# Kernel optimization log

Hardware: AMD Instinct MI355X
Metric: run time of the kernel (lower is better)

Reference implementation:

```python
import jax, jax.numpy as jnp
import numpy as np

N_NODES = 100000
N_EDGES = 3200000
NODE_DIM = 128
HIDDEN = 16


def setup_inputs() -> dict:
    key = jax.random.key(0)
    ks = jax.random.split(key, 12)
    x = jax.random.normal(ks[0], (N_NODES, NODE_DIM), dtype=jnp.float32)
    edge_src = jax.random.randint(ks[1], (N_EDGES,), 0, N_NODES, dtype=jnp.int32)
    edge_dst = jax.random.randint(ks[2], (N_EDGES,), 0, N_NODES, dtype=jnp.int32)
    # QCNN block params (Linear(node_dim,16), Linear(16,16), Linear(16,16)) + classifier Linear(16,1)
    s1 = 1.0 / np.sqrt(NODE_DIM)
    s2 = 1.0 / np.sqrt(HIDDEN)
    W1 = jax.random.uniform(ks[3], (NODE_DIM, HIDDEN), jnp.float32, -s1, s1)
    b1 = jax.random.uniform(ks[4], (HIDDEN,), jnp.float32, -s1, s1)
    W2 = jax.random.uniform(ks[5], (HIDDEN, HIDDEN), jnp.float32, -s2, s2)
    b2 = jax.random.uniform(ks[6], (HIDDEN,), jnp.float32, -s2, s2)
    W3 = jax.random.uniform(ks[7], (HIDDEN, HIDDEN), jnp.float32, -s2, s2)
    b3 = jax.random.uniform(ks[8], (HIDDEN,), jnp.float32, -s2, s2)
    Wc = jax.random.uniform(ks[9], (HIDDEN, 1), jnp.float32, -s2, s2)
    bc = jax.random.uniform(ks[10], (1,), jnp.float32, -s2, s2)
    return {"x": x, "edge_src": edge_src, "edge_dst": edge_dst,
            "W1": W1, "b1": b1, "W2": W2, "b2": b2, "W3": W3, "b3": b3,
            "Wc": Wc, "bc": bc}


def reference(x, edge_src, edge_dst, W1, b1, W2, b2, W3, b3, Wc, bc):
    # per-node tiny 3-layer tanh MLP (QCNN block), vectorized over all nodes
    h = jnp.tanh(x @ W1 + b1)
    h = jnp.tanh(h @ W2 + b2)
    h = jnp.tanh(h @ W3 + b3)  # [N, H]
    n = x.shape[0]
    # degree of each aggregating node; nodes with no neighbors contribute 0
    deg = jnp.zeros((n,), x.dtype).at[edge_src].add(1.0)
    inv_deg = jnp.where(deg > 0, 1.0 / jnp.maximum(deg, 1.0), 0.0)
    # aggregated = sum_n mean_{m in N(n)} h[m] = sum_e h[dst_e] / deg[src_e]
    agg = jnp.sum(h[edge_dst] * inv_deg[edge_src][:, None], axis=0) / n  # [H]
    return jax.nn.sigmoid(agg @ Wc + bc)  # [1]
```

## Files before the change

### kernel.cpp

```cpp
#include <hip/hip_runtime.h>
#include <math.h>


#define NODE_DIM 128
#define HID 16

typedef __attribute__((ext_vector_type(8))) short    bfrag8;
typedef __attribute__((ext_vector_type(4))) _Float16 hfrag4;
typedef __attribute__((ext_vector_type(4))) float    f32x4;

__device__ __forceinline__ float fast_tanh(float x) {
    x = fminf(fmaxf(x, -10.0f), 10.0f);
    float e = __expf(2.0f * x);
    return (e - 1.0f) * __frcp_rn(e + 1.0f);
}
__device__ __forceinline__ unsigned short f2bf(float f) {
    unsigned u = __float_as_uint(f);
    return (unsigned short)((u + 0x7FFFu + ((u >> 16) & 1u)) >> 16);
}

__global__ __launch_bounds__(256) void k_mlp(
    const float* __restrict__ x,
    const float* __restrict__ W1, const float* __restrict__ b1,
    const float* __restrict__ W2, const float* __restrict__ b2,
    const float* __restrict__ W3, const float* __restrict__ b3,
    const float* __restrict__ Wc,
    unsigned char* __restrict__ c_code, int n_nodes)
{
    const int lane = threadIdx.x & 63;
    const int col  = lane & 15;
    const int q    = lane >> 4;

    bfrag8 w1f[4];
#pragma unroll
    for (int kc = 0; kc < 4; ++kc)
#pragma unroll
        for (int j = 0; j < 8; ++j)
            w1f[kc][j] = (short)f2bf(W1[(kc * 32 + q * 8 + j) * HID + col]);

    hfrag4 w2t, w3t;
#pragma unroll
    for (int j = 0; j < 4; ++j) {
        w2t[j] = (_Float16)W2[(q * 4 + j) * HID + col];
        w3t[j] = (_Float16)W3[(q * 4 + j) * HID + col];
    }
    float bb1[4], bb2[4], bb3[4], wcr[4];
#pragma unroll
    for (int j = 0; j < 4; ++j) {
        bb1[j] = b1[q * 4 + j]; bb2[j] = b2[q * 4 + j];
        bb3[j] = b3[q * 4 + j]; wcr[j] = Wc[q * 4 + j];
    }

    const int ngroups = (n_nodes + 15) >> 4;
    const int nwaves  = gridDim.x * (blockDim.x >> 6);
    const int wgid    = (blockIdx.x * blockDim.x + threadIdx.x) >> 6;
    const f32x4 zero = {0.f, 0.f, 0.f, 0.f};

    for (int g = wgid; g < ngroups; g += nwaves) {
        const int node0 = g << 4;
        int m = node0 + col;
        int mload = (m < n_nodes) ? m : (n_nodes - 1);
        const float* xr = x + (size_t)mload * NODE_DIM;

        float4 xa[4], xb[4];
#pragma unroll
        for (int kc = 0; kc < 4; ++kc) {
            const float* p = xr + kc * 32 + q * 8;
            xa[kc] = *reinterpret_cast<const float4*>(p);
            xb[kc] = *reinterpret_cast<const float4*>(p + 4);
        }
        f32x4 d1 = zero;
#pragma unroll
        for (int kc = 0; kc < 4; ++kc) {
            bfrag8 bf;
            bf[0] = (short)f2bf(xa[kc].x); bf[1] = (short)f2bf(xa[kc].y);
            bf[2] = (short)f2bf(xa[kc].z); bf[3] = (short)f2bf(xa[kc].w);
            bf[4] = (short)f2bf(xb[kc].x); bf[5] = (short)f2bf(xb[kc].y);
            bf[6] = (short)f2bf(xb[kc].z); bf[7] = (short)f2bf(xb[kc].w);
            d1 = __builtin_amdgcn_mfma_f32_16x16x32_bf16(w1f[kc], bf, d1, 0, 0, 0);
        }
        hfrag4 h1;
#pragma unroll
        for (int r = 0; r < 4; ++r) h1[r] = (_Float16)fast_tanh(d1[r] + bb1[r]);

        f32x4 d2 = __builtin_amdgcn_mfma_f32_16x16x16f16(w2t, h1, zero, 0, 0, 0);
        hfrag4 h2;
#pragma unroll
        for (int r = 0; r < 4; ++r) h2[r] = (_Float16)fast_tanh(d2[r] + bb2[r]);

        f32x4 d3 = __builtin_amdgcn_mfma_f32_16x16x16f16(w3t, h2, zero, 0, 0, 0);

        float v = 0.0f;
#pragma unroll
        for (int r = 0; r < 4; ++r) v += fast_tanh(d3[r] + bb3[r]) * wcr[r];
        v += __shfl_xor(v, 16, 64);
        v += __shfl_xor(v, 32, 64);

        if (lane < 16) {
            const int node = node0 + lane;
            if (node < n_nodes) {
                float c = fminf(fmaxf(v, -4.0f), 4.0f);
                c_code[node] = (unsigned char)__float2int_rn((c + 4.0f) * 16.0f);
            }
        }
    }
}

__global__ __launch_bounds__(1024) void k_gaccum(
    const int* __restrict__ src, const int* __restrict__ dst,
    const unsigned char* __restrict__ c_code,
    unsigned int* __restrict__ tables,
    float* __restrict__ gtotal, unsigned int* __restrict__ ticket,
    int n_edges, int ch, int n_chunks, int n_slices)
{
    extern __shared__ unsigned char dynlds[];
    unsigned int* tab = (unsigned int*)dynlds;
    const int tid   = threadIdx.x;
    const int chunk = blockIdx.x % n_chunks;
    const int slice = blockIdx.x / n_chunks;
    const int lo    = chunk * ch;
    const int words = ch >> 1;

    if (blockIdx.x == 0 && tid == 0) { *gtotal = 0.0f; *ticket = 0u; }

    uint4* t4 = reinterpret_cast<uint4*>(tab);
    const uint4 z4 = {0u, 0u, 0u, 0u};
    for (int i = tid; i < (words >> 2); i += 1024) t4[i] = z4;
    __syncthreads();

    const int epb = ((n_edges + n_slices - 1) / n_slices + 7) & ~7;
    const int e0 = slice * epb;
    const int e1 = min(e0 + epb, n_edges);

    for (int e = e0 + (tid << 3); e < e1; e += 1024 * 8) {
        if (e + 7 < e1) {
            int4 s0 = *reinterpret_cast<const int4*>(src + e);
            int4 s1 = *reinterpret_cast<const int4*>(src + e + 4);
            int4 d0 = *reinterpret_cast<const int4*>(dst + e);
            int4 d1 = *reinterpret_cast<const int4*>(dst + e + 4);
            unsigned c0 = c_code[d0.x], c1 = c_code[d0.y];
            unsigned c2 = c_code[d0.z], c3 = c_code[d0.w];
            unsigned c4 = c_code[d1.x], c5 = c_code[d1.y];
            unsigned c6 = c_code[d1.z], c7 = c_code[d1.w];
            int i0 = s0.x - lo, i1 = s0.y - lo, i2 = s0.z - lo, i3 = s0.w - lo;
            int i4 = s1.x - lo, i5 = s1.y - lo, i6 = s1.z - lo, i7 = s1.w - lo;
            if ((unsigned)i0 < (unsigned)ch) atomicAdd(&tab[i0 >> 1], ((1u << 12) | c0) << ((i0 & 1) << 4));
            if ((unsigned)i1 < (unsigned)ch) atomicAdd(&tab[i1 >> 1], ((1u << 12) | c1) << ((i1 & 1) << 4));
            if ((unsigned)i2 < (unsigned)ch) atomicAdd(&tab[i2 >> 1], ((1u << 12) | c2) << ((i2 & 1) << 4));
            if ((unsigned)i3 < (unsigned)ch) atomicAdd(&tab[i3 >> 1], ((1u << 12) | c3) << ((i3 & 1) << 4));
            if ((unsigned)i4 < (unsigned)ch) atomicAdd(&tab[i4 >> 1], ((1u << 12) | c4) << ((i4 & 1) << 4));
            if ((unsigned)i5 < (unsigned)ch) atomicAdd(&tab[i5 >> 1], ((1u << 12) | c5) << ((i5 & 1) << 4));
            if ((unsigned)i6 < (unsigned)ch) atomicAdd(&tab[i6 >> 1], ((1u << 12) | c6) << ((i6 & 1) << 4));
            if ((unsigned)i7 < (unsigned)ch) atomicAdd(&tab[i7 >> 1], ((1u << 12) | c7) << ((i7 & 1) << 4));
        } else {
            for (int j = e; j < e1; ++j) {
                int ss = src[j] - lo;
                if ((unsigned)ss < (unsigned)ch)
                    atomicAdd(&tab[ss >> 1],
                              ((1u << 12) | (unsigned)c_code[dst[j]]) << ((ss & 1) << 4));
            }
        }
    }
    __syncthreads();
    uint4* out4 = reinterpret_cast<uint4*>(tables + (size_t)(slice * n_chunks + chunk) * words);
    for (int i = tid; i < (words >> 2); i += 1024) out4[i] = t4[i];
}

__global__ __launch_bounds__(256) void k_totalfinal(
    const unsigned int* __restrict__ tables, const float* __restrict__ bc,
    float* __restrict__ out, float* __restrict__ gtotal,
    unsigned int* __restrict__ ticket,
    int n_chunks, int ch, int n_slices, float inv_n, int ntb)
{
    __shared__ float swave[4];
    const int wpc = ch >> 1;
    const int wg  = blockIdx.x * blockDim.x + threadIdx.x;
    const int chunk = wg / wpc, w = wg - chunk * wpc;
    const unsigned int stride = (unsigned int)(n_chunks * wpc);
    const unsigned int base0  = (unsigned int)(chunk * wpc + w);

    unsigned int sfix = 0, scnt = 0;
    for (int s = 0; s < n_slices; s += 8) {
        unsigned int v[8];
#pragma unroll
        for (int k = 0; k < 8; ++k)
            v[k] = tables[(size_t)(s + k) * stride + base0];
#pragma unroll
        for (int k = 0; k < 8; ++k) {
            sfix += v[k] & 0x0FFF0FFFu;
            scnt += (v[k] >> 12) & 0x000F000Fu;
        }
    }
    const unsigned int cnt_lo = scnt & 0xFFFFu, cnt_hi = scnt >> 16;
    const unsigned int fix_lo = sfix & 0xFFFFu, fix_hi = sfix >> 16;
    float contrib = 0.0f;
    if (cnt_lo > 0) contrib += (float)fix_lo / (16.0f * (float)cnt_lo) - 4.0f;
    if (cnt_hi > 0) contrib += (float)fix_hi / (16.0f * (float)cnt_hi) - 4.0f;

    for (int off = 32; off > 0; off >>= 1) contrib += __shfl_down(contrib, off, 64);
    if ((threadIdx.x & 63) == 0) swave[threadIdx.x >> 6] = contrib;
    __syncthreads();
    if (threadIdx.x == 0) {
        float part = swave[0] + swave[1] + swave[2] + swave[3];
        atomicAdd(gtotal, part);
        __threadfence();
        unsigned int t = atomicAdd(ticket, 1u);
        if (t == (unsigned int)(ntb - 1)) {
            __threadfence();
            float tot = atomicAdd(gtotal, 0.0f);
            float sv = tot * inv_n + bc[0];
            out[0] = 1.0f / (1.0f + __expf(-sv));
        }
    }
}

extern "C" void kernel_launch(void* const* d_in, const int* in_sizes, int n_in,
                              void* d_out, int out_size, void* d_ws, size_t ws_size,
                              hipStream_t stream) {
    const float* x   = (const float*)d_in[0];
    const int* esrc  = (const int*)d_in[1];
    const int* edst  = (const int*)d_in[2];
    const float* W1  = (const float*)d_in[3];
    const float* b1  = (const float*)d_in[4];
    const float* W2  = (const float*)d_in[5];
    const float* b2  = (const float*)d_in[6];
    const float* W3  = (const float*)d_in[7];
    const float* b3  = (const float*)d_in[8];
    const float* Wc  = (const float*)d_in[9];
    const float* bc  = (const float*)d_in[10];

    const int n_nodes = in_sizes[0] / NODE_DIM;
    const int n_edges = in_sizes[1];

    bool big = true;
    if (hipFuncSetAttribute((const void*)k_gaccum,
            hipFuncAttributeMaxDynamicSharedMemorySize, 131072) != hipSuccess) big = false;

    const int ch_a  = big ? 50176 : 32768;
    const int nch_a = (n_nodes + ch_a - 1) / ch_a;
    const int nsl   = 128;
    const int words = ch_a >> 1;

    const size_t tab_b = (size_t)nsl * nch_a * words * 4;
    unsigned int* tables  = (unsigned int*)d_ws;
    float* gtotal         = (float*)((char*)d_ws + tab_b);
    unsigned int* ticket  = (unsigned int*)(gtotal + 1);
    unsigned char* c_code = (unsigned char*)d_ws + tab_b + 16;

    k_mlp<<<512, 256, 0, stream>>>(x, W1, b1, W2, b2, W3, b3, Wc, c_code, n_nodes);

    k_gaccum<<<nsl * nch_a, 1024, (size_t)ch_a * 2, stream>>>(
        esrc, edst, c_code, tables, gtotal, ticket, n_edges, ch_a, nch_a, nsl);

    const int ntb = (nch_a * words) / 256;
    k_totalfinal<<<ntb, 256, 0, stream>>>(
        tables, bc, (float*)d_out, gtotal, ticket,
        nch_a, ch_a, nsl, 1.0f / (float)n_nodes, ntb);
}
```

Measured before the change: 152.6 us.

## Replace sliced LDS histogram tables with direct global per-node atomics

The chunked LDS histogram, which wrote 128 per-slice partial tables to global memory and then reduced them, is replaced by one packed 32-bit word per node (count in the upper half, quantized code sum in the lower half). Edges update these words with global atomics, and the final kernel reads one word per node. Zeroing of that table moves into the MLP kernel, which now launches one wave per 16-node group and issues the x loads before the weight loads. This removes the large partial-table write and readback, and the repeated edge scans per chunk. In exchange, all updates become random global atomics that contend in L2.

```diff
diff --git a/kernel.cpp b/kernel.cpp
--- a/kernel.cpp
+++ b/kernel.cpp
@@ -25,12 +25,39 @@
     const float* __restrict__ W2, const float* __restrict__ b2,
     const float* __restrict__ W3, const float* __restrict__ b3,
     const float* __restrict__ Wc,
-    unsigned char* __restrict__ c_code, int n_nodes)
+    unsigned char* __restrict__ c_code,
+    unsigned int* __restrict__ ntab,
+    float* __restrict__ gtotal, unsigned int* __restrict__ ticket,
+    int n_nodes)
 {
+    {
+        const int gsz = gridDim.x * blockDim.x;
+        for (int i = blockIdx.x * blockDim.x + threadIdx.x; i < n_nodes; i += gsz)
+            ntab[i] = 0u;
+        if (blockIdx.x == 0 && threadIdx.x == 0) { *gtotal = 0.0f; *ticket = 0u; }
+    }
+
     const int lane = threadIdx.x & 63;
     const int col  = lane & 15;
     const int q    = lane >> 4;
 
+    const int ngroups = (n_nodes + 15) >> 4;
+    const int wgid    = (blockIdx.x * blockDim.x + threadIdx.x) >> 6;
+    if (wgid >= ngroups) return;
+
+    const int node0 = wgid << 4;
+    int m = node0 + col;
+    int mload = (m < n_nodes) ? m : (n_nodes - 1);
+    const float* xr = x + (size_t)mload * NODE_DIM;
+
+    float4 xa[4], xb[4];
+#pragma unroll
+    for (int kc = 0; kc < 4; ++kc) {
+        const float* p = xr + kc * 32 + q * 8;
+        xa[kc] = *reinterpret_cast<const float4*>(p);
+        xb[kc] = *reinterpret_cast<const float4*>(p + 4);
+    }
+
     bfrag8 w1f[4];
 #pragma unroll
     for (int kc = 0; kc < 4; ++kc)
@@ -51,151 +78,90 @@
         bb3[j] = b3[q * 4 + j]; wcr[j] = Wc[q * 4 + j];
     }
 
-    const int ngroups = (n_nodes + 15) >> 4;
-    const int nwaves  = gridDim.x * (blockDim.x >> 6);
-    const int wgid    = (blockIdx.x * blockDim.x + threadIdx.x) >> 6;
     const f32x4 zero = {0.f, 0.f, 0.f, 0.f};
-
-    for (int g = wgid; g < ngroups; g += nwaves) {
-        const int node0 = g << 4;
-        int m = node0 + col;
-        int mload = (m < n_nodes) ? m : (n_nodes - 1);
-        const float* xr = x + (size_t)mload * NODE_DIM;
-
-        float4 xa[4], xb[4];
-#pragma unroll
-        for (int kc = 0; kc < 4; ++kc) {
-            const float* p = xr + kc * 32 + q * 8;
-            xa[kc] = *reinterpret_cast<const float4*>(p);
-            xb[kc] = *reinterpret_cast<const float4*>(p + 4);
+    f32x4 d1 = zero;
+#pragma unroll
+    for (int kc = 0; kc < 4; ++kc) {
+        bfrag8 bf;
+        bf[0] = (short)f2bf(xa[kc].x); bf[1] = (short)f2bf(xa[kc].y);
+        bf[2] = (short)f2bf(xa[kc].z); bf[3] = (short)f2bf(xa[kc].w);
+        bf[4] = (short)f2bf(xb[kc].x); bf[5] = (short)f2bf(xb[kc].y);
+        bf[6] = (short)f2bf(xb[kc].z); bf[7] = (short)f2bf(xb[kc].w);
+        d1 = __builtin_amdgcn_mfma_f32_16x16x32_bf16(w1f[kc], bf, d1, 0, 0, 0);
+    }
+    hfrag4 h1;
+#pragma unroll
+    for (int r = 0; r < 4; ++r) h1[r] = (_Float16)fast_tanh(d1[r] + bb1[r]);
+
+    f32x4 d2 = __builtin_amdgcn_mfma_f32_16x16x16f16(w2t, h1, zero, 0, 0, 0);
+    hfrag4 h2;
+#pragma unroll
+    for (int r = 0; r < 4; ++r) h2[r] = (_Float16)fast_tanh(d2[r] + bb2[r]);
+
+    f32x4 d3 = __builtin_amdgcn_mfma_f32_16x16x16f16(w3t, h2, zero, 0, 0, 0);
+
+    float v = 0.0f;
+#pragma unroll
+    for (int r = 0; r < 4; ++r) v += fast_tanh(d3[r] + bb3[r]) * wcr[r];
+    v += __shfl_xor(v, 16, 64);
+    v += __shfl_xor(v, 32, 64);
+
+    if (lane < 16) {
+        const int node = node0 + lane;
+        if (node < n_nodes) {
+            float c = fminf(fmaxf(v, -4.0f), 4.0f);
+            c_code[node] = (unsigned char)__float2int_rn((c + 4.0f) * 16.0f);
         }
-        f32x4 d1 = zero;
-#pragma unroll
-        for (int kc = 0; kc < 4; ++kc) {
-            bfrag8 bf;
-            bf[0] = (short)f2bf(xa[kc].x); bf[1] = (short)f2bf(xa[kc].y);
-            bf[2] = (short)f2bf(xa[kc].z); bf[3] = (short)f2bf(xa[kc].w);
-            bf[4] = (short)f2bf(xb[kc].x); bf[5] = (short)f2bf(xb[kc].y);
-            bf[6] = (short)f2bf(xb[kc].z); bf[7] = (short)f2bf(xb[kc].w);
-            d1 = __builtin_amdgcn_mfma_f32_16x16x32_bf16(w1f[kc], bf, d1, 0, 0, 0);
-        }
-        hfrag4 h1;
-#pragma unroll
-        for (int r = 0; r < 4; ++r) h1[r] = (_Float16)fast_tanh(d1[r] + bb1[r]);
-
-        f32x4 d2 = __builtin_amdgcn_mfma_f32_16x16x16f16(w2t, h1, zero, 0, 0, 0);
-        hfrag4 h2;
-#pragma unroll
-        for (int r = 0; r < 4; ++r) h2[r] = (_Float16)fast_tanh(d2[r] + bb2[r]);
-
-        f32x4 d3 = __builtin_amdgcn_mfma_f32_16x16x16f16(w3t, h2, zero, 0, 0, 0);
-
-        float v = 0.0f;
-#pragma unroll
-        for (int r = 0; r < 4; ++r) v += fast_tanh(d3[r] + bb3[r]) * wcr[r];
-        v += __shfl_xor(v, 16, 64);
-        v += __shfl_xor(v, 32, 64);
-
-        if (lane < 16) {
-            const int node = node0 + lane;
-            if (node < n_nodes) {
-                float c = fminf(fmaxf(v, -4.0f), 4.0f);
-                c_code[node] = (unsigned char)__float2int_rn((c + 4.0f) * 16.0f);
-            }
-        }
-    }
-}
-
-__global__ __launch_bounds__(1024) void k_gaccum(
+    }
+}
+
+__global__ __launch_bounds__(256) void k_edge(
     const int* __restrict__ src, const int* __restrict__ dst,
     const unsigned char* __restrict__ c_code,
-    unsigned int* __restrict__ tables,
-    float* __restrict__ gtotal, unsigned int* __restrict__ ticket,
-    int n_edges, int ch, int n_chunks, int n_slices)
+    unsigned int* __restrict__ ntab, int n_edges)
 {
-    extern __shared__ unsigned char dynlds[];
-    unsigned int* tab = (unsigned int*)dynlds;
-    const int tid   = threadIdx.x;
-    const int chunk = blockIdx.x % n_chunks;
-    const int slice = blockIdx.x / n_chunks;
-    const int lo    = chunk * ch;
-    const int words = ch >> 1;
-
-    if (blockIdx.x == 0 && tid == 0) { *gtotal = 0.0f; *ticket = 0u; }
-
-    uint4* t4 = reinterpret_cast<uint4*>(tab);
-    const uint4 z4 = {0u, 0u, 0u, 0u};
-    for (int i = tid; i < (words >> 2); i += 1024) t4[i] = z4;
-    __syncthreads();
-
-    const int epb = ((n_edges + n_slices - 1) / n_slices + 7) & ~7;
-    const int e0 = slice * epb;
-    const int e1 = min(e0 + epb, n_edges);
-
-    for (int e = e0 + (tid << 3); e < e1; e += 1024 * 8) {
-        if (e + 7 < e1) {
-            int4 s0 = *reinterpret_cast<const int4*>(src + e);
-            int4 s1 = *reinterpret_cast<const int4*>(src + e + 4);
-            int4 d0 = *reinterpret_cast<const int4*>(dst + e);
-            int4 d1 = *reinterpret_cast<const int4*>(dst + e + 4);
-            unsigned c0 = c_code[d0.x], c1 = c_code[d0.y];
-            unsigned c2 = c_code[d0.z], c3 = c_code[d0.w];
-            unsigned c4 = c_code[d1.x], c5 = c_code[d1.y];
-            unsigned c6 = c_code[d1.z], c7 = c_code[d1.w];
-            int i0 = s0.x - lo, i1 = s0.y - lo, i2 = s0.z - lo, i3 = s0.w - lo;
-            int i4 = s1.x - lo, i5 = s1.y - lo, i6 = s1.z - lo, i7 = s1.w - lo;
-            if ((unsigned)i0 < (unsigned)ch) atomicAdd(&tab[i0 >> 1], ((1u << 12) | c0) << ((i0 & 1) << 4));
-            if ((unsigned)i1 < (unsigned)ch) atomicAdd(&tab[i1 >> 1], ((1u << 12) | c1) << ((i1 & 1) << 4));
-            if ((unsigned)i2 < (unsigned)ch) atomicAdd(&tab[i2 >> 1], ((1u << 12) | c2) << ((i2 & 1) << 4));
-            if ((unsigned)i3 < (unsigned)ch) atomicAdd(&tab[i3 >> 1], ((1u << 12) | c3) << ((i3 & 1) << 4));
-            if ((unsigned)i4 < (unsigned)ch) atomicAdd(&tab[i4 >> 1], ((1u << 12) | c4) << ((i4 & 1) << 4));
-            if ((unsigned)i5 < (unsigned)ch) atomicAdd(&tab[i5 >> 1], ((1u << 12) | c5) << ((i5 & 1) << 4));
-            if ((unsigned)i6 < (unsigned)ch) atomicAdd(&tab[i6 >> 1], ((1u << 12) | c6) << ((i6 & 1) << 4));
-            if ((unsigned)i7 < (unsigned)ch) atomicAdd(&tab[i7 >> 1], ((1u << 12) | c7) << ((i7 & 1) << 4));
-        } else {
-            for (int j = e; j < e1; ++j) {
-                int ss = src[j] - lo;
-                if ((unsigned)ss < (unsigned)ch)
-                    atomicAdd(&tab[ss >> 1],
-                              ((1u << 12) | (unsigned)c_code[dst[j]]) << ((ss & 1) << 4));
-            }
-        }
-    }
-    __syncthreads();
-    uint4* out4 = reinterpret_cast<uint4*>(tables + (size_t)(slice * n_chunks + chunk) * words);
-    for (int i = tid; i < (words >> 2); i += 1024) out4[i] = t4[i];
-}
-
-__global__ __launch_bounds__(256) void k_totalfinal(
-    const unsigned int* __restrict__ tables, const float* __restrict__ bc,
+    const int t  = blockIdx.x * blockDim.x + threadIdx.x;
+    const int e  = t << 3;
+    if (e >= n_edges) return;
+
+    if (e + 7 < n_edges) {
+        int4 s0 = *reinterpret_cast<const int4*>(src + e);
+        int4 s1 = *reinterpret_cast<const int4*>(src + e + 4);
+        int4 d0 = *reinterpret_cast<const int4*>(dst + e);
+        int4 d1 = *reinterpret_cast<const int4*>(dst + e + 4);
+        unsigned c0 = c_code[d0.x], c1 = c_code[d0.y];
+        unsigned c2 = c_code[d0.z], c3 = c_code[d0.w];
+        unsigned c4 = c_code[d1.x], c5 = c_code[d1.y];
+        unsigned c6 = c_code[d1.z], c7 = c_code[d1.w];
+        atomicAdd(&ntab[s0.x], 0x10000u | c0);
+        atomicAdd(&ntab[s0.y], 0x10000u | c1);
+        atomicAdd(&ntab[s0.z], 0x10000u | c2);
+        atomicAdd(&ntab[s0.w], 0x10000u | c3);
+        atomicAdd(&ntab[s1.x], 0x10000u | c4);
+        atomicAdd(&ntab[s1.y], 0x10000u | c5);
+        atomicAdd(&ntab[s1.z], 0x10000u | c6);
+        atomicAdd(&ntab[s1.w], 0x10000u | c7);
+    } else {
+        for (int j = e; j < n_edges; ++j)
+            atomicAdd(&ntab[src[j]], 0x10000u | (unsigned)c_code[dst[j]]);
+    }
+}
+
+__global__ __launch_bounds__(256) void k_final(
+    const unsigned int* __restrict__ ntab, const float* __restrict__ bc,
     float* __restrict__ out, float* __restrict__ gtotal,
     unsigned int* __restrict__ ticket,
-    int n_chunks, int ch, int n_slices, float inv_n, int ntb)
+    int n_nodes, float inv_n, int nblocks)
 {
     __shared__ float swave[4];
-    const int wpc = ch >> 1;
-    const int wg  = blockIdx.x * blockDim.x + threadIdx.x;
-    const int chunk = wg / wpc, w = wg - chunk * wpc;
-    const unsigned int stride = (unsigned int)(n_chunks * wpc);
-    const unsigned int base0  = (unsigned int)(chunk * wpc + w);
-
-    unsigned int sfix = 0, scnt = 0;
-    for (int s = 0; s < n_slices; s += 8) {
-        unsigned int v[8];
-#pragma unroll
-        for (int k = 0; k < 8; ++k)
-            v[k] = tables[(size_t)(s + k) * stride + base0];
-#pragma unroll
-        for (int k = 0; k < 8; ++k) {
-            sfix += v[k] & 0x0FFF0FFFu;
-            scnt += (v[k] >> 12) & 0x000F000Fu;
-        }
-    }
-    const unsigned int cnt_lo = scnt & 0xFFFFu, cnt_hi = scnt >> 16;
-    const unsigned int fix_lo = sfix & 0xFFFFu, fix_hi = sfix >> 16;
+    const int i = blockIdx.x * blockDim.x + threadIdx.x;
+
     float contrib = 0.0f;
-    if (cnt_lo > 0) contrib += (float)fix_lo / (16.0f * (float)cnt_lo) - 4.0f;
-    if (cnt_hi > 0) contrib += (float)fix_hi / (16.0f * (float)cnt_hi) - 4.0f;
+    if (i < n_nodes) {
+        unsigned int w = ntab[i];
+        unsigned int cnt = w >> 16, fix = w & 0xFFFFu;
+        if (cnt > 0) contrib = (float)fix / (16.0f * (float)cnt) - 4.0f;
+    }
 
     for (int off = 32; off > 0; off >>= 1) contrib += __shfl_down(contrib, off, 64);
     if ((threadIdx.x & 63) == 0) swave[threadIdx.x >> 6] = contrib;
@@ -205,7 +171,7 @@
         atomicAdd(gtotal, part);
         __threadfence();
         unsigned int t = atomicAdd(ticket, 1u);
-        if (t == (unsigned int)(ntb - 1)) {
+        if (t == (unsigned int)(nblocks - 1)) {
             __threadfence();
             float tot = atomicAdd(gtotal, 0.0f);
             float sv = tot * inv_n + bc[0];
@@ -232,28 +198,21 @@
     const int n_nodes = in_sizes[0] / NODE_DIM;
     const int n_edges = in_sizes[1];
 
-    bool big = true;
-    if (hipFuncSetAttribute((const void*)k_gaccum,
-            hipFuncAttributeMaxDynamicSharedMemorySize, 131072) != hipSuccess) big = false;
-
-    const int ch_a  = big ? 50176 : 32768;
-    const int nch_a = (n_nodes + ch_a - 1) / ch_a;
-    const int nsl   = 128;
-    const int words = ch_a >> 1;
-
-    const size_t tab_b = (size_t)nsl * nch_a * words * 4;
-    unsigned int* tables  = (unsigned int*)d_ws;
-    float* gtotal         = (float*)((char*)d_ws + tab_b);
+    unsigned int* ntab    = (unsigned int*)d_ws;
+    float* gtotal         = (float*)(ntab + n_nodes);
     unsigned int* ticket  = (unsigned int*)(gtotal + 1);
-    unsigned char* c_code = (unsigned char*)d_ws + tab_b + 16;
-
-    k_mlp<<<512, 256, 0, stream>>>(x, W1, b1, W2, b2, W3, b3, Wc, c_code, n_nodes);
-
-    k_gaccum<<<nsl * nch_a, 1024, (size_t)ch_a * 2, stream>>>(
-        esrc, edst, c_code, tables, gtotal, ticket, n_edges, ch_a, nch_a, nsl);
-
-    const int ntb = (nch_a * words) / 256;
-    k_totalfinal<<<ntb, 256, 0, stream>>>(
-        tables, bc, (float*)d_out, gtotal, ticket,
-        nch_a, ch_a, nsl, 1.0f / (float)n_nodes, ntb);
-}
+    unsigned char* c_code = (unsigned char*)d_ws + (size_t)n_nodes * 4 + 16;
+
+    const int ngroups = (n_nodes + 15) >> 4;
+    const int mlp_wg  = (ngroups + 3) >> 2;
+    k_mlp<<<mlp_wg, 256, 0, stream>>>(x, W1, b1, W2, b2, W3, b3, Wc,
+                                      c_code, ntab, gtotal, ticket, n_nodes);
+
+    const int edge_blocks = (((n_edges + 7) >> 3) + 255) >> 8;
+    k_edge<<<edge_blocks, 256, 0, stream>>>(esrc, edst, c_code, ntab, n_edges);
+
+    const int fin_blocks = (n_nodes + 255) >> 8;
+    k_final<<<fin_blocks, 256, 0, stream>>>(ntab, bc, (float*)d_out,
+                                            gtotal, ticket, n_nodes,
+                                            1.0f / (float)n_nodes, fin_blocks);
+}
```

Result: slower. 261.3 us (+71.2%).

## Stage node codes in LDS for edge pass and retile chunks and slices

Applied to the files above, without the earlier changes.

The edge accumulation kernel now copies the whole per-node byte code array (about 100KB) into LDS, so the random gathers by dst index hit LDS instead of global memory or L2. To make room, LDS is raised to 160KB and the source-node range is split into 4 chunks × 64 slices, which also changes the partial-table layout. The MLP kernel becomes one-shot with one 16-node group per wave instead of a grid-stride loop, and the zeroing of gtotal and ticket moves into it. The tradeoff is that every block reloads the full code array, and occupancy is limited to one block per CU because of the large LDS footprint.

```diff
diff --git a/kernel.cpp b/kernel.cpp
--- a/kernel.cpp
+++ b/kernel.cpp
@@ -25,12 +25,33 @@
     const float* __restrict__ W2, const float* __restrict__ b2,
     const float* __restrict__ W3, const float* __restrict__ b3,
     const float* __restrict__ Wc,
-    unsigned char* __restrict__ c_code, int n_nodes)
+    unsigned char* __restrict__ c_code,
+    float* __restrict__ gtotal, unsigned int* __restrict__ ticket,
+    int n_nodes)
 {
+    if (blockIdx.x == 0 && threadIdx.x == 0) { *gtotal = 0.0f; *ticket = 0u; }
+
     const int lane = threadIdx.x & 63;
     const int col  = lane & 15;
     const int q    = lane >> 4;
 
+    const int ngroups = (n_nodes + 15) >> 4;
+    const int wgid    = (blockIdx.x * blockDim.x + threadIdx.x) >> 6;
+    if (wgid >= ngroups) return;
+
+    const int node0 = wgid << 4;
+    int m = node0 + col;
+    int mload = (m < n_nodes) ? m : (n_nodes - 1);
+    const float* xr = x + (size_t)mload * NODE_DIM;
+
+    float4 xa[4], xb[4];
+#pragma unroll
+    for (int kc = 0; kc < 4; ++kc) {
+        const float* p = xr + kc * 32 + q * 8;
+        xa[kc] = *reinterpret_cast<const float4*>(p);
+        xb[kc] = *reinterpret_cast<const float4*>(p + 4);
+    }
+
     bfrag8 w1f[4];
 #pragma unroll
     for (int kc = 0; kc < 4; ++kc)
@@ -51,78 +72,61 @@
         bb3[j] = b3[q * 4 + j]; wcr[j] = Wc[q * 4 + j];
     }
 
-    const int ngroups = (n_nodes + 15) >> 4;
-    const int nwaves  = gridDim.x * (blockDim.x >> 6);
-    const int wgid    = (blockIdx.x * blockDim.x + threadIdx.x) >> 6;
     const f32x4 zero = {0.f, 0.f, 0.f, 0.f};
-
-    for (int g = wgid; g < ngroups; g += nwaves) {
-        const int node0 = g << 4;
-        int m = node0 + col;
-        int mload = (m < n_nodes) ? m : (n_nodes - 1);
-        const float* xr = x + (size_t)mload * NODE_DIM;
-
-        float4 xa[4], xb[4];
-#pragma unroll
-        for (int kc = 0; kc < 4; ++kc) {
-            const float* p = xr + kc * 32 + q * 8;
-            xa[kc] = *reinterpret_cast<const float4*>(p);
-            xb[kc] = *reinterpret_cast<const float4*>(p + 4);
-        }
-        f32x4 d1 = zero;
-#pragma unroll
-        for (int kc = 0; kc < 4; ++kc) {
-            bfrag8 bf;
-            bf[0] = (short)f2bf(xa[kc].x); bf[1] = (short)f2bf(xa[kc].y);
-            bf[2] = (short)f2bf(xa[kc].z); bf[3] = (short)f2bf(xa[kc].w);
-            bf[4] = (short)f2bf(xb[kc].x); bf[5] = (short)f2bf(xb[kc].y);
-            bf[6] = (short)f2bf(xb[kc].z); bf[7] = (short)f2bf(xb[kc].w);
-            d1 = __builtin_amdgcn_mfma_f32_16x16x32_bf16(w1f[kc], bf, d1, 0, 0, 0);
-        }
-        hfrag4 h1;
-#pragma unroll
-        for (int r = 0; r < 4; ++r) h1[r] = (_Float16)fast_tanh(d1[r] + bb1[r]);
-
-        f32x4 d2 = __builtin_amdgcn_mfma_f32_16x16x16f16(w2t, h1, zero, 0, 0, 0);
-        hfrag4 h2;
-#pragma unroll
-        for (int r = 0; r < 4; ++r) h2[r] = (_Float16)fast_tanh(d2[r] + bb2[r]);
-
-        f32x4 d3 = __builtin_amdgcn_mfma_f32_16x16x16f16(w3t, h2, zero, 0, 0, 0);
-
-        float v = 0.0f;
-#pragma unroll
-        for (int r = 0; r < 4; ++r) v += fast_tanh(d3[r] + bb3[r]) * wcr[r];
-        v += __shfl_xor(v, 16, 64);
-        v += __shfl_xor(v, 32, 64);
-
-        if (lane < 16) {
-            const int node = node0 + lane;
-            if (node < n_nodes) {
-                float c = fminf(fmaxf(v, -4.0f), 4.0f);
-                c_code[node] = (unsigned char)__float2int_rn((c + 4.0f) * 16.0f);
-            }
-        }
-    }
-}
-
-__global__ __launch_bounds__(1024) void k_gaccum(
+    f32x4 d1 = zero;
+#pragma unroll
+    for (int kc = 0; kc < 4; ++kc) {
+        bfrag8 bf;
+        bf[0] = (short)f2bf(xa[kc].x); bf[1] = (short)f2bf(xa[kc].y);
+        bf[2] = (short)f2bf(xa[kc].z); bf[3] = (short)f2bf(xa[kc].w);
+        bf[4] = (short)f2bf(xb[kc].x); bf[5] = (short)f2bf(xb[kc].y);
+        bf[6] = (short)f2bf(xb[kc].z); bf[7] = (short)f2bf(xb[kc].w);
+        d1 = __builtin_amdgcn_mfma_f32_16x16x32_bf16(w1f[kc], bf, d1, 0, 0, 0);
+    }
+    hfrag4 h1;
+#pragma unroll
+    for (int r = 0; r < 4; ++r) h1[r] = (_Float16)fast_tanh(d1[r] + bb1[r]);
+
+    f32x4 d2 = __builtin_amdgcn_mfma_f32_16x16x16f16(w2t, h1, zero, 0, 0, 0);
+    hfrag4 h2;
+#pragma unroll
+    for (int r = 0; r < 4; ++r) h2[r] = (_Float16)fast_tanh(d2[r] + bb2[r]);
+
+    f32x4 d3 = __builtin_amdgcn_mfma_f32_16x16x16f16(w3t, h2, zero, 0, 0, 0);
+
+    float v = 0.0f;
+#pragma unroll
+    for (int r = 0; r < 4; ++r) v += fast_tanh(d3[r] + bb3[r]) * wcr[r];
+    v += __shfl_xor(v, 16, 64);
+    v += __shfl_xor(v, 32, 64);
+
+    if (lane < 16) {
+        const int node = node0 + lane;
+        if (node < n_nodes) {
+            float c = fminf(fmaxf(v, -4.0f), 4.0f);
+            c_code[node] = (unsigned char)__float2int_rn((c + 4.0f) * 16.0f);
+        }
+    }
+}
+
+__global__ __launch_bounds__(1024) void k_edge1(
     const int* __restrict__ src, const int* __restrict__ dst,
     const unsigned char* __restrict__ c_code,
     unsigned int* __restrict__ tables,
-    float* __restrict__ gtotal, unsigned int* __restrict__ ticket,
-    int n_edges, int ch, int n_chunks, int n_slices)
+    int n_edges, int ch, int n_chunks, int n_slices, int code_bytes)
 {
     extern __shared__ unsigned char dynlds[];
-    unsigned int* tab = (unsigned int*)dynlds;
+    unsigned char* scode = dynlds;
+    unsigned int*  tab   = (unsigned int*)(dynlds + code_bytes);
     const int tid   = threadIdx.x;
     const int chunk = blockIdx.x % n_chunks;
     const int slice = blockIdx.x / n_chunks;
     const int lo    = chunk * ch;
     const int words = ch >> 1;
 
-    if (blockIdx.x == 0 && tid == 0) { *gtotal = 0.0f; *ticket = 0u; }
-
+    const unsigned int* cp = reinterpret_cast<const unsigned int*>(c_code);
+    unsigned int* scp = reinterpret_cast<unsigned int*>(scode);
+    for (int i = tid; i < (code_bytes >> 2); i += 1024) scp[i] = cp[i];
     uint4* t4 = reinterpret_cast<uint4*>(tab);
     const uint4 z4 = {0u, 0u, 0u, 0u};
     for (int i = tid; i < (words >> 2); i += 1024) t4[i] = z4;
@@ -138,10 +142,10 @@
             int4 s1 = *reinterpret_cast<const int4*>(src + e + 4);
             int4 d0 = *reinterpret_cast<const int4*>(dst + e);
             int4 d1 = *reinterpret_cast<const int4*>(dst + e + 4);
-            unsigned c0 = c_code[d0.x], c1 = c_code[d0.y];
-            unsigned c2 = c_code[d0.z], c3 = c_code[d0.w];
-            unsigned c4 = c_code[d1.x], c5 = c_code[d1.y];
-            unsigned c6 = c_code[d1.z], c7 = c_code[d1.w];
+            unsigned c0 = scode[d0.x], c1 = scode[d0.y];
+            unsigned c2 = scode[d0.z], c3 = scode[d0.w];
+            unsigned c4 = scode[d1.x], c5 = scode[d1.y];
+            unsigned c6 = scode[d1.z], c7 = scode[d1.w];
             int i0 = s0.x - lo, i1 = s0.y - lo, i2 = s0.z - lo, i3 = s0.w - lo;
             int i4 = s1.x - lo, i5 = s1.y - lo, i6 = s1.z - lo, i7 = s1.w - lo;
             if ((unsigned)i0 < (unsigned)ch) atomicAdd(&tab[i0 >> 1], ((1u << 12) | c0) << ((i0 & 1) << 4));
@@ -157,7 +161,7 @@
                 int ss = src[j] - lo;
                 if ((unsigned)ss < (unsigned)ch)
                     atomicAdd(&tab[ss >> 1],
-                              ((1u << 12) | (unsigned)c_code[dst[j]]) << ((ss & 1) << 4));
+                              ((1u << 12) | (unsigned)scode[dst[j]]) << ((ss & 1) << 4));
             }
         }
     }
@@ -232,28 +236,37 @@
     const int n_nodes = in_sizes[0] / NODE_DIM;
     const int n_edges = in_sizes[1];
 
-    bool big = true;
-    if (hipFuncSetAttribute((const void*)k_gaccum,
-            hipFuncAttributeMaxDynamicSharedMemorySize, 131072) != hipSuccess) big = false;
-
-    const int ch_a  = big ? 50176 : 32768;
-    const int nch_a = (n_nodes + ch_a - 1) / ch_a;
-    const int nsl   = 128;
-    const int words = ch_a >> 1;
-
-    const size_t tab_b = (size_t)nsl * nch_a * words * 4;
+    const int code_bytes = (n_nodes + 1023) & ~1023;
+
+    int nch, nsl;
+    if (hipFuncSetAttribute((const void*)k_edge1,
+            hipFuncAttributeMaxDynamicSharedMemorySize, 163840) == hipSuccess) {
+        nch = 4; nsl = 64;
+    } else {
+        (void)hipFuncSetAttribute((const void*)k_edge1,
+            hipFuncAttributeMaxDynamicSharedMemorySize, 131072);
+        nch = 8; nsl = 32;
+    }
+    const int ch    = code_bytes / nch;
+    const int words = ch >> 1;
+    const size_t lds_b = (size_t)code_bytes + (size_t)ch * 2;
+
+    const size_t tab_b = (size_t)nsl * nch * words * 4;
     unsigned int* tables  = (unsigned int*)d_ws;
     float* gtotal         = (float*)((char*)d_ws + tab_b);
     unsigned int* ticket  = (unsigned int*)(gtotal + 1);
     unsigned char* c_code = (unsigned char*)d_ws + tab_b + 16;
 
-    k_mlp<<<512, 256, 0, stream>>>(x, W1, b1, W2, b2, W3, b3, Wc, c_code, n_nodes);
-
-    k_gaccum<<<nsl * nch_a, 1024, (size_t)ch_a * 2, stream>>>(
-        esrc, edst, c_code, tables, gtotal, ticket, n_edges, ch_a, nch_a, nsl);
-
-    const int ntb = (nch_a * words) / 256;
+    const int ngroups = (n_nodes + 15) >> 4;
+    const int mlp_wg  = (ngroups + 3) >> 2;
+    k_mlp<<<mlp_wg, 256, 0, stream>>>(x, W1, b1, W2, b2, W3, b3, Wc,
+                                      c_code, gtotal, ticket, n_nodes);
+
+    k_edge1<<<nch * nsl, 1024, lds_b, stream>>>(
+        esrc, edst, c_code, tables, n_edges, ch, nch, nsl, code_bytes);
+
+    const int ntb = (nch * words) / 256;
     k_totalfinal<<<ntb, 256, 0, stream>>>(
         tables, bc, (float*)d_out, gtotal, ticket,
-        nch_a, ch_a, nsl, 1.0f / (float)n_nodes, ntb);
-}
+        nch, ch, nsl, 1.0f / (float)n_nodes, ntb);
+}
```

Result: faster. 148.6 us (-2.6%).
